# Optimization experiments

Hardware: AMD Instinct MI355X
Metric: run time of the kernel (lower is better)

The kernel has to match this reference:

```python
import jax, jax.numpy as jnp
import numpy as np
import math

N_COARSE, N_FINE = 8192, 32768
DEC_DIM, ENC_DIM, OUT_DIM, K = 256, 128, 128, 16
LN_EPS = 1e-5


def setup_inputs() -> dict:
    key = jax.random.key(0)
    ks = jax.random.split(key, 16)
    s = lambda fan_in: 1.0 / math.sqrt(fan_in)
    return {
        "decoder_features": jax.random.normal(ks[0], (N_COARSE, DEC_DIM), jnp.float32),
        "decoder_pos": jax.random.normal(ks[1], (N_COARSE, 3), jnp.float32),
        "encoder_features": jax.random.normal(ks[2], (N_FINE, ENC_DIM), jnp.float32),
        "encoder_pos": jax.random.normal(ks[3], (N_FINE, 3), jnp.float32),
        "encoder_labels": jax.random.randint(ks[4], (N_FINE,), 0, 13, jnp.int64),
        # params (torch nn.Linear default init scale)
        "Wq": jax.random.uniform(ks[5], (DEC_DIM, ENC_DIM), jnp.float32, -s(ENC_DIM), s(ENC_DIM)),
        "bq": jnp.zeros((DEC_DIM,), jnp.float32),
        "Wk": jax.random.uniform(ks[6], (DEC_DIM, DEC_DIM), jnp.float32, -s(DEC_DIM), s(DEC_DIM)),
        "bk": jnp.zeros((DEC_DIM,), jnp.float32),
        "Wv": jax.random.uniform(ks[7], (DEC_DIM, DEC_DIM), jnp.float32, -s(DEC_DIM), s(DEC_DIM)),
        "bv": jnp.zeros((DEC_DIM,), jnp.float32),
        "W1": jax.random.uniform(ks[8], (OUT_DIM, DEC_DIM + ENC_DIM), jnp.float32, -s(DEC_DIM + ENC_DIM), s(DEC_DIM + ENC_DIM)),
        "b1": jnp.zeros((OUT_DIM,), jnp.float32),
        "W2": jax.random.uniform(ks[9], (OUT_DIM, OUT_DIM), jnp.float32, -s(OUT_DIM), s(OUT_DIM)),
        "b2": jnp.zeros((OUT_DIM,), jnp.float32),
        "ln_g": jnp.ones((OUT_DIM,), jnp.float32),
        "ln_b": jnp.zeros((OUT_DIM,), jnp.float32),
    }


def _knn_indices(encoder_pos, decoder_pos, k):
    # For each fine (encoder) point, k nearest coarse (decoder) points.
    # squared distances [N_fine, N_coarse]
    d2 = (
        jnp.sum(encoder_pos * encoder_pos, axis=1, keepdims=True)
        - 2.0 * encoder_pos @ decoder_pos.T
        + jnp.sum(decoder_pos * decoder_pos, axis=1)[None, :]
    )
    _, idx = jax.lax.top_k(-d2, k)  # [N_fine, K]
    return idx


def reference(decoder_features, decoder_pos, encoder_features, encoder_pos,
              encoder_labels, Wq, bq, Wk, bk, Wv, bv, W1, b1, W2, b2, ln_g, ln_b):
    idx = _knn_indices(encoder_pos, decoder_pos, K)            # [Nf, K]
    nbr = decoder_features[idx]                                 # [Nf, K, Dd]
    query = encoder_features @ Wq.T + bq                        # [Nf, Dd]
    keys = nbr @ Wk.T + bk                                      # [Nf, K, Dd]
    values = nbr @ Wv.T + bv                                    # [Nf, K, Dd]
    scores = jnp.einsum('nd,nkd->nk', query, keys) / math.sqrt(DEC_DIM)
    # segment softmax over edges grouped by fine target == softmax over K
    weights = jax.nn.softmax(scores, axis=-1)                   # [Nf, K]
    agg = jnp.einsum('nk,nkd->nd', weights, values)             # [Nf, Dd]
    combined = jnp.concatenate([agg, encoder_features], axis=-1)
    h = jax.nn.relu(combined @ W1.T + b1)
    up = h @ W2.T + b2                                          # [Nf, out]
    mu = jnp.mean(up, axis=-1, keepdims=True)
    var = jnp.var(up, axis=-1, keepdims=True)
    out = (up - mu) * jax.lax.rsqrt(var + LN_EPS) * ln_g + ln_b
    # dropout is identity in eval mode
    return (out, encoder_pos, encoder_labels)
```

## Files before the change

### kernel.cpp

```cpp
#include <hip/hip_runtime.h>
#include <hip/hip_bf16.h>

typedef __hip_bfloat16 bf16;
typedef unsigned short u16;
typedef float f32x2 __attribute__((ext_vector_type(2)));

#define NC 8192
#define NF 32768
#define KNN 16
#define FMAXV 3.402823466e+38f

__device__ __forceinline__ float bfbits2f(u16 u){
  union { unsigned u; float f; } x; x.u = ((unsigned)u) << 16; return x.f;
}
__device__ __forceinline__ float asfloat(unsigned u){
  union { unsigned u; float f; } x; x.u = u; return x.f;
}
__device__ __forceinline__ f32x2 pk_fma(f32x2 a, f32x2 b, f32x2 c){
  f32x2 d;
  asm("v_pk_fma_f32 %0, %1, %2, %3" : "=v"(d) : "v"(a), "v"(b), "v"(c));
  return d;
}

__global__ __launch_bounds__(256) void k_prep(const float* __restrict__ dpos,
                                              const float* __restrict__ W1,
                                              const float* __restrict__ W2,
                                              float4* __restrict__ posP,
                                              float4* __restrict__ W1eSa,
                                              float4* __restrict__ W1eSb,
                                              float4* __restrict__ W2Sa,
                                              float4* __restrict__ W2Sb){
  int g = blockIdx.x * 256 + threadIdx.x;
  if (g < 4096){
    const float2* dp2 = (const float2*)(dpos + (size_t)g * 6);
    float2 a = dp2[0], b = dp2[1], c = dp2[2];
    float x0 = a.x, y0 = a.y, z0 = b.x;
    float x1 = b.y, y1 = c.x, z1 = c.y;
    float dd0 = __fadd_rn(__fadd_rn(__fmul_rn(x0,x0), __fmul_rn(y0,y0)), __fmul_rn(z0,z0));
    float dd1 = __fadd_rn(__fadd_rn(__fmul_rn(x1,x1), __fmul_rn(y1,y1)), __fmul_rn(z1,z1));
    posP[g * 2]     = make_float4(x0, x1, y0, y1);
    posP[g * 2 + 1] = make_float4(z0, z1, dd0 * 0.5f, dd1 * 0.5f);
  } else if (g >= 8192 && g < 10240){
    int f = g - 8192; int c4 = f >> 6, jg = f & 63;
    W1eSa[f] = ((const float4*)(W1 + (size_t)(2 * jg) * 384 + 256))[c4];
  } else if (g >= 10240 && g < 12288){
    int f = g - 10240; int c4 = f >> 6, jg = f & 63;
    W1eSb[f] = ((const float4*)(W1 + (size_t)(2 * jg + 1) * 384 + 256))[c4];
  } else if (g >= 12288 && g < 14336){
    int f = g - 12288; int c4 = f >> 6, jg = f & 63;
    W2Sa[f] = ((const float4*)(W2 + (size_t)(2 * jg) * 128))[c4];
  } else if (g >= 14336){
    int f = g - 14336; int c4 = f >> 6, jg = f & 63;
    W2Sb[f] = ((const float4*)(W2 + (size_t)(2 * jg + 1) * 128))[c4];
  }
}

__global__ __launch_bounds__(256) void k_wprod(const float* __restrict__ Wk,
                                               const float* __restrict__ Wv,
                                               const float* __restrict__ Wq,
                                               const float* __restrict__ W1,
                                               const float* __restrict__ bk,
                                               const float* __restrict__ bv,
                                               const float* __restrict__ bq,
                                               float* __restrict__ WkqS,
                                               float* __restrict__ WvuS,
                                               float* __restrict__ bkq,
                                               float* __restrict__ bvu,
                                               float* __restrict__ wbq,
                                               float* __restrict__ sbq){
  __shared__ float partial[256];
  __shared__ float red[256];
  int B = blockIdx.x, t = threadIdx.x;
  int csel = B >> 2, tch = B & 3;
  int o = (t & 63) + tch * 64;
  int q = t >> 6;
  int j0 = q * 64;
  if (csel < 128){
    int c = csel;
    float acc = 0.f;
    for (int j = j0; j < j0 + 64; ++j)
      acc = fmaf(Wk[(size_t)j * 256 + o], Wq[(size_t)j * 128 + c], acc);
    partial[t] = acc;
    if (tch == 0) red[t] = bk[t] * Wq[(size_t)t * 128 + c];
    __syncthreads();
    if (t < 64){
      float a = partial[t] + partial[t + 64] + partial[t + 128] + partial[t + 192];
      WkqS[(size_t)((o >> 2) * 128 + c) * 4 + (o & 3)] = a;
    }
    if (tch == 0){
      for (int s = 128; s > 0; s >>= 1){ if (t < s) red[t] += red[t + s]; __syncthreads(); }
      if (t == 0) bkq[c] = red[0];
    }
  } else if (csel < 256){
    int h = csel - 128;
    float acc = 0.f;
    for (int j = j0; j < j0 + 64; ++j)
      acc = fmaf(Wv[(size_t)j * 256 + o], W1[(size_t)h * 384 + j], acc);
    partial[t] = acc;
    if (tch == 0) red[t] = bv[t] * W1[(size_t)h * 384 + t];
    __syncthreads();
    if (t < 64){
      float a = partial[t] + partial[t + 64] + partial[t + 128] + partial[t + 192];
      WvuS[(size_t)((o >> 2) * 128 + h) * 4 + (o & 3)] = a;
    }
    if (tch == 0){
      for (int s = 128; s > 0; s >>= 1){ if (t < s) red[t] += red[t + s]; __syncthreads(); }
      if (t == 0) bvu[h] = red[0];
    }
  } else {
    float acc = 0.f;
    for (int j = j0; j < j0 + 64; ++j)
      acc = fmaf(Wk[(size_t)j * 256 + o], bq[j], acc);
    partial[t] = acc;
    if (tch == 0) red[t] = bk[t] * bq[t];
    __syncthreads();
    if (t < 64){
      float a = partial[t] + partial[t + 64] + partial[t + 128] + partial[t + 192];
      wbq[o] = a;
    }
    if (tch == 0){
      for (int s = 128; s > 0; s >>= 1){ if (t < s) red[t] += red[t + s]; __syncthreads(); }
      if (t == 0) sbq[0] = red[0];
    }
  }
}

__global__ __launch_bounds__(256) void k_dec(const float* __restrict__ df,
                                             const float4* __restrict__ WkqS,
                                             const float4* __restrict__ WvuS,
                                             const float* __restrict__ bkq,
                                             const float* __restrict__ bvu,
                                             const float* __restrict__ wbq,
                                             const float* __restrict__ sbq,
                                             bf16* __restrict__ Zd, bf16* __restrict__ Ud,
                                             float* __restrict__ bqK){
  __shared__ float part[8][32];
  int t = threadIdx.x;
  int g0 = blockIdx.x * 8;
  int half = __builtin_amdgcn_readfirstlane(t >> 7);
  int c = t & 127;
  const float4* W = half ? WvuS : WkqS;
  float acc[8];
  #pragma unroll
  for (int p = 0; p < 8; ++p) acc[p] = 0.f;
  for (int j4 = 0; j4 < 64; ++j4){
    float4 w = W[j4 * 128 + c];
    #pragma unroll
    for (int p = 0; p < 8; ++p){
      float4 a = ((const float4*)(df + (size_t)(g0 + p) * 256))[j4];
      acc[p] += w.x*a.x + w.y*a.y + w.z*a.z + w.w*a.w;
    }
  }
  float bias = half ? bvu[c] : bkq[c];
  bf16* dst = half ? Ud : Zd;
  #pragma unroll
  for (int p = 0; p < 8; ++p)
    dst[(size_t)(g0 + p) * 128 + c] = __float2bfloat16(acc[p] + bias);
  {
    int r = t >> 5, seg = t & 31;
    float s = 0.f;
    const float* dr = df + (size_t)(g0 + r) * 256 + seg * 8;
    const float* wq = wbq + seg * 8;
    #pragma unroll
    for (int e = 0; e < 8; ++e) s = fmaf(dr[e], wq[e], s);
    part[r][seg] = s;
  }
  __syncthreads();
  if (t < 8){
    float s = sbq[0];
    #pragma unroll
    for (int seg = 0; seg < 32; ++seg) s += part[t][seg];
    bqK[g0 + t] = s;
  }
}

__global__ __launch_bounds__(128) void k_attn(const float* __restrict__ epos,
                                              const float4* __restrict__ posP,
                                              const float* __restrict__ ef,
                                              const bf16* __restrict__ Zd,
                                              const bf16* __restrict__ Ud,
                                              const float* __restrict__ bqK,
                                              bf16* __restrict__ hagg){
  __shared__ float lval[2][8][64];
  __shared__ int   lidx[2][8][64];
  __shared__ int   cntL[2][8];

  int t = threadIdx.x, lane = t & 63, w = t >> 6;
  int n0 = blockIdx.x * 16 + w * 8;

  f32x2 nex2[8], ney2[8], nez2[8];
  #pragma unroll
  for (int p = 0; p < 8; ++p){
    float nx = -epos[(n0 + p) * 3 + 0];
    float ny = -epos[(n0 + p) * 3 + 1];
    float nz = -epos[(n0 + p) * 3 + 2];
    nex2[p].x = nx; nex2[p].y = nx;
    ney2[p].x = ny; ney2[p].y = ny;
    nez2[p].x = nz; nez2[p].y = nz;
  }

  f32x2 vmin2[8];
  #pragma unroll
  for (int p = 0; p < 8; ++p){ vmin2[p].x = FMAXV; vmin2[p].y = FMAXV; }
  #pragma unroll 2
  for (int s = 0; s < 64; ++s){
    int q2 = (s * 64 + lane) * 2;
    float4 XY = posP[q2], ZW = posP[q2 + 1];
    f32x2 X = {XY.x, XY.y}, Y = {XY.z, XY.w}, Z = {ZW.x, ZW.y}, W = {ZW.z, ZW.w};
    #pragma unroll
    for (int p = 0; p < 8; ++p){
      f32x2 v2 = pk_fma(nex2[p], X, W);
      v2 = pk_fma(ney2[p], Y, v2);
      v2 = pk_fma(nez2[p], Z, v2);
      vmin2[p].x = fminf(vmin2[p].x, v2.x);
      vmin2[p].y = fminf(vmin2[p].y, v2.y);
    }
  }
  float vmin[8];
  #pragma unroll
  for (int p = 0; p < 8; ++p) vmin[p] = fminf(vmin2[p].x, vmin2[p].y);

  #pragma unroll
  for (int k = 2; k <= 64; k <<= 1){
    #pragma unroll
    for (int j = k >> 1; j > 0; j >>= 1){
      bool keepmin = ((lane & j) == 0) == ((lane & k) == 0);
      #pragma unroll
      for (int p = 0; p < 8; ++p){
        float pv = __shfl_xor(vmin[p], j);
        vmin[p] = keepmin ? fminf(vmin[p], pv) : fmaxf(vmin[p], pv);
      }
    }
  }
  float tau0[8];
  #pragma unroll
  for (int p = 0; p < 8; ++p) tau0[p] = __shfl(vmin[p], 16);

  unsigned long long lmlt = (1ull << lane) - 1ull;
  int cnt[8] = {0,0,0,0,0,0,0,0};
  #pragma unroll 2
  for (int s = 0; s < 64; ++s){
    int q = s * 64 + lane;
    float4 XY = posP[q * 2], ZW = posP[q * 2 + 1];
    f32x2 X = {XY.x, XY.y}, Y = {XY.z, XY.w}, Z = {ZW.x, ZW.y}, W = {ZW.z, ZW.w};
    int cand0 = q * 2;
    #pragma unroll
    for (int p = 0; p < 8; ++p){
      f32x2 v2 = pk_fma(nex2[p], X, W);
      v2 = pk_fma(ney2[p], Y, v2);
      v2 = pk_fma(nez2[p], Z, v2);
      bool h0 = v2.x <= tau0[p];
      bool h1 = v2.y <= tau0[p];
      if (__any(h0 || h1)){
        unsigned long long m0 = __ballot(h0);
        unsigned long long m1 = __ballot(h1);
        int base = cnt[p];
        int c0 = __popcll(m0);
        if (h0){
          int s0 = base + (int)__popcll(m0 & lmlt);
          if (s0 < 64){ lval[w][p][s0] = v2.x; lidx[w][p][s0] = cand0; }
        }
        if (h1){
          int s1 = base + c0 + (int)__popcll(m1 & lmlt);
          if (s1 < 64){ lval[w][p][s1] = v2.y; lidx[w][p][s1] = cand0 + 1; }
        }
        cnt[p] = base + c0 + (int)__popcll(m1);
      }
    }
  }
  if (lane == 0){
    #pragma unroll
    for (int p = 0; p < 8; ++p) cntL[w][p] = cnt[p];
  }
  __syncthreads();

  #pragma unroll 1
  for (int u = 0; u < 4; ++u){
    int p0 = u * 2, p1 = u * 2 + 1;
    int nA = n0 + p0, nB = n0 + p1;
    int c0 = cntL[w][p0]; if (c0 > 64) c0 = 64;
    int c1 = cntL[w][p1]; if (c1 > 64) c1 = 64;
    float va = (lane < c0) ? lval[w][p0][lane] : FMAXV;
    int   ia = (lane < c0) ? lidx[w][p0][lane] : 0x7fffffff;
    float vb = (lane < c1) ? lval[w][p1][lane] : FMAXV;
    int   ib = (lane < c1) ? lidx[w][p1][lane] : 0x7fffffff;

    #pragma unroll
    for (int k = 2; k <= 16; k <<= 1){
      #pragma unroll
      for (int j = k >> 1; j > 0; j >>= 1){
        bool keepmin = ((lane & k) == 0) == ((lane & j) == 0);
        { float pv = __shfl_xor(va, j); int pid = __shfl_xor(ia, j);
          bool pl = (pv < va) || (pv == va && pid < ia);
          if (keepmin ? pl : !pl){ va = pv; ia = pid; } }
        { float pv = __shfl_xor(vb, j); int pid = __shfl_xor(ib, j);
          bool pl = (pv < vb) || (pv == vb && pid < ib);
          if (keepmin ? pl : !pl){ vb = pv; ib = pid; } }
      }
    }
    { float pv = __shfl_xor(va, 16); int pid = __shfl_xor(ia, 16);
      if ((pv < va) || (pv == va && pid < ia)){ va = pv; ia = pid; } }
    { float pv = __shfl_xor(vb, 16); int pid = __shfl_xor(ib, 16);
      if ((pv < vb) || (pv == vb && pid < ib)){ vb = pv; ib = pid; } }
    #pragma unroll
    for (int j = 8; j > 0; j >>= 1){
      bool keepmin = ((lane & 32) == 0) == ((lane & j) == 0);
      { float pv = __shfl_xor(va, j); int pid = __shfl_xor(ia, j);
        bool pl = (pv < va) || (pv == va && pid < ia);
        if (keepmin ? pl : !pl){ va = pv; ia = pid; } }
      { float pv = __shfl_xor(vb, j); int pid = __shfl_xor(ib, j);
        bool pl = (pv < vb) || (pv == vb && pid < ib);
        if (keepmin ? pl : !pl){ vb = pv; ib = pid; } }
    }
    { float pv = __shfl_xor(va, 32); int pid = __shfl_xor(ia, 32);
      if ((pv < va) || (pv == va && pid < ia)){ va = pv; ia = pid; } }
    { float pv = __shfl_xor(vb, 32); int pid = __shfl_xor(ib, 32);
      if ((pv < vb) || (pv == vb && pid < ib)){ vb = pv; ib = pid; } }
    int topi0 = ia, topi1 = ib;

    int kk = lane & 15, part = lane >> 4;
    int ik0 = __shfl(topi0, kk);
    int ik1 = __shfl(topi1, kk);
    const uint4*  zr0 = (const uint4*)((const u16*)Zd + (size_t)ik0 * 128) + part * 4;
    const uint4*  zr1 = (const uint4*)((const u16*)Zd + (size_t)ik1 * 128) + part * 4;
    const float4* e40 = (const float4*)(ef + (size_t)nA * 128) + part * 8;
    const float4* e41 = (const float4*)(ef + (size_t)nB * 128) + part * 8;
    float pr0 = 0.f, pr1 = 0.f;
    #pragma unroll
    for (int i = 0; i < 4; ++i){
      uint4 z0 = zr0[i], z1 = zr1[i];
      float4 ea0 = e40[2 * i], eb0 = e40[2 * i + 1];
      float4 ea1 = e41[2 * i], eb1 = e41[2 * i + 1];
      pr0 = fmaf(ea0.x, asfloat(z0.x << 16), pr0); pr0 = fmaf(ea0.y, asfloat(z0.x & 0xffff0000u), pr0);
      pr0 = fmaf(ea0.z, asfloat(z0.y << 16), pr0); pr0 = fmaf(ea0.w, asfloat(z0.y & 0xffff0000u), pr0);
      pr0 = fmaf(eb0.x, asfloat(z0.z << 16), pr0); pr0 = fmaf(eb0.y, asfloat(z0.z & 0xffff0000u), pr0);
      pr0 = fmaf(eb0.z, asfloat(z0.w << 16), pr0); pr0 = fmaf(eb0.w, asfloat(z0.w & 0xffff0000u), pr0);
      pr1 = fmaf(ea1.x, asfloat(z1.x << 16), pr1); pr1 = fmaf(ea1.y, asfloat(z1.x & 0xffff0000u), pr1);
      pr1 = fmaf(ea1.z, asfloat(z1.y << 16), pr1); pr1 = fmaf(ea1.w, asfloat(z1.y & 0xffff0000u), pr1);
      pr1 = fmaf(eb1.x, asfloat(z1.z << 16), pr1); pr1 = fmaf(eb1.y, asfloat(z1.z & 0xffff0000u), pr1);
      pr1 = fmaf(eb1.z, asfloat(z1.w << 16), pr1); pr1 = fmaf(eb1.w, asfloat(z1.w & 0xffff0000u), pr1);
    }
    pr0 += __shfl_xor(pr0, 16); pr1 += __shfl_xor(pr1, 16);
    pr0 += __shfl_xor(pr0, 32); pr1 += __shfl_xor(pr1, 32);
    float sc0 = (pr0 + bqK[ik0]) * (1.0f / 16.0f);
    float sc1 = (pr1 + bqK[ik1]) * (1.0f / 16.0f);

    float mx0 = sc0, mx1 = sc1;
    #pragma unroll
    for (int off = 8; off >= 1; off >>= 1){
      mx0 = fmaxf(mx0, __shfl_xor(mx0, off));
      mx1 = fmaxf(mx1, __shfl_xor(mx1, off));
    }
    float e0 = (lane < KNN) ? __expf(sc0 - mx0) : 0.f;
    float e1 = (lane < KNN) ? __expf(sc1 - mx1) : 0.f;
    float l0 = e0, l1 = e1;
    #pragma unroll
    for (int off = 8; off >= 1; off >>= 1){
      l0 += __shfl_xor(l0, off);
      l1 += __shfl_xor(l1, off);
    }
    float wgt0 = (lane < KNN) ? (e0 / l0) : 0.f;
    float wgt1 = (lane < KNN) ? (e1 / l1) : 0.f;

    float a00 = 0.f, a01 = 0.f, a10 = 0.f, a11 = 0.f;
    #pragma unroll
    for (int k = 0; k < KNN; ++k){
      int ikk0 = __shfl(topi0, k);
      int ikk1 = __shfl(topi1, k);
      float wk0 = __shfl(wgt0, k);
      float wk1 = __shfl(wgt1, k);
      ushort2 u0 = *(const ushort2*)((const u16*)Ud + (size_t)ikk0 * 128 + lane * 2);
      ushort2 u1 = *(const ushort2*)((const u16*)Ud + (size_t)ikk1 * 128 + lane * 2);
      a00 = fmaf(wk0, bfbits2f(u0.x), a00);
      a01 = fmaf(wk0, bfbits2f(u0.y), a01);
      a10 = fmaf(wk1, bfbits2f(u1.x), a10);
      a11 = fmaf(wk1, bfbits2f(u1.y), a11);
    }
    bf16 h00 = __float2bfloat16(a00), h01 = __float2bfloat16(a01);
    bf16 h10 = __float2bfloat16(a10), h11 = __float2bfloat16(a11);
    ushort2 st0; st0.x = *(u16*)&h00; st0.y = *(u16*)&h01;
    ushort2 st1; st1.x = *(u16*)&h10; st1.y = *(u16*)&h11;
    *(ushort2*)(hagg + (size_t)nA * 128 + lane * 2) = st0;
    *(ushort2*)(hagg + (size_t)nB * 128 + lane * 2) = st1;
  }
}

__global__ __launch_bounds__(256) void k_mlp(const bf16* __restrict__ hagg,
                                             const float* __restrict__ ef,
                                             const float4* __restrict__ W1eSa,
                                             const float4* __restrict__ W1eSb,
                                             const float* __restrict__ b1,
                                             const float4* __restrict__ W2Sa,
                                             const float4* __restrict__ W2Sb,
                                             const float* __restrict__ b2,
                                             const float* __restrict__ lng, const float* __restrict__ lnb,
                                             const float* __restrict__ epos, const int* __restrict__ lab,
                                             float* __restrict__ out){
  __shared__ float hbuf[16 * 128];
  __shared__ float ubuf[16 * 128];
  __shared__ float stats[32];
  int t = threadIdx.x;
  int n0 = blockIdx.x * 16;
  {
    int gid = blockIdx.x * 256 + t;
    if (gid < NF){
      float* op = out + (size_t)NF * 128;
      op[gid * 3 + 0] = epos[gid * 3 + 0];
      op[gid * 3 + 1] = epos[gid * 3 + 1];
      op[gid * 3 + 2] = epos[gid * 3 + 2];
      out[(size_t)NF * 128 + (size_t)NF * 3 + gid] = (float)lab[gid];
    }
  }
  int jg = t & 63;
  int pg4 = __builtin_amdgcn_readfirstlane((t >> 6) * 4);
  int j0 = jg * 2;
  float acc[2][4];
  #pragma unroll
  for (int a = 0; a < 2; ++a)
    #pragma unroll
    for (int p = 0; p < 4; ++p) acc[a][p] = 0.f;
  for (int c4 = 0; c4 < 32; ++c4){
    float4 wa = W1eSa[c4 * 64 + jg];
    float4 wb = W1eSb[c4 * 64 + jg];
    #pragma unroll
    for (int p = 0; p < 4; ++p){
      float4 x = ((const float4*)(ef + (size_t)(n0 + pg4 + p) * 128))[c4];
      acc[0][p] += wa.x*x.x + wa.y*x.y + wa.z*x.z + wa.w*x.w;
      acc[1][p] += wb.x*x.x + wb.y*x.y + wb.z*x.z + wb.w*x.w;
    }
  }
  float b1a = b1[j0], b1b = b1[j0 + 1];
  #pragma unroll
  for (int p = 0; p < 4; ++p){
    size_t row = (size_t)(n0 + pg4 + p);
    ushort2 hgv = *(const ushort2*)((const u16*)hagg + row * 128 + j0);
    hbuf[(pg4 + p) * 128 + j0]     = fmaxf(acc[0][p] + b1a + bfbits2f(hgv.x), 0.f);
    hbuf[(pg4 + p) * 128 + j0 + 1] = fmaxf(acc[1][p] + b1b + bfbits2f(hgv.y), 0.f);
  }
  __syncthreads();
  float acc2[2][4];
  #pragma unroll
  for (int a = 0; a < 2; ++a)
    #pragma unroll
    for (int p = 0; p < 4; ++p) acc2[a][p] = 0.f;
  const float4* hb4 = (const float4*)hbuf;
  for (int c4 = 0; c4 < 32; ++c4){
    float4 wa = W2Sa[c4 * 64 + jg];
    float4 wb = W2Sb[c4 * 64 + jg];
    #pragma unroll
    for (int p = 0; p < 4; ++p){
      float4 x = hb4[(pg4 + p) * 32 + c4];
      acc2[0][p] += wa.x*x.x + wa.y*x.y + wa.z*x.z + wa.w*x.w;
      acc2[1][p] += wb.x*x.x + wb.y*x.y + wb.z*x.z + wb.w*x.w;
    }
  }
  float b2a = b2[j0], b2b = b2[j0 + 1];
  float u[2][4];
  #pragma unroll
  for (int p = 0; p < 4; ++p){
    u[0][p] = acc2[0][p] + b2a;
    u[1][p] = acc2[1][p] + b2b;
    ubuf[(pg4 + p) * 128 + j0]     = u[0][p];
    ubuf[(pg4 + p) * 128 + j0 + 1] = u[1][p];
  }
  __syncthreads();
  {
    int p = t >> 4, qi = t & 15;
    const float* ub = &ubuf[p * 128 + qi * 8];
    float s = 0.f, s2 = 0.f;
    #pragma unroll
    for (int e2i = 0; e2i < 8; ++e2i){ float v = ub[e2i]; s += v; s2 += v * v; }
    #pragma unroll
    for (int off = 1; off < 16; off <<= 1){ s += __shfl_xor(s, off); s2 += __shfl_xor(s2, off); }
    if (qi == 0){
      float mu = s * (1.f / 128.f);
      float var = s2 * (1.f / 128.f) - mu * mu;
      stats[p] = mu;
      stats[16 + p] = rsqrtf(fmaxf(var, 0.f) + 1e-5f);
    }
  }
  __syncthreads();
  float ga = lng[j0], gb = lng[j0 + 1];
  float ba = lnb[j0], bbv = lnb[j0 + 1];
  #pragma unroll
  for (int p = 0; p < 4; ++p){
    float mu = stats[pg4 + p], rs = stats[16 + pg4 + p];
    out[(size_t)(n0 + pg4 + p) * 128 + j0]     = (u[0][p] - mu) * rs * ga + ba;
    out[(size_t)(n0 + pg4 + p) * 128 + j0 + 1] = (u[1][p] - mu) * rs * gb + bbv;
  }
}

extern "C" void kernel_launch(void* const* d_in, const int* in_sizes, int n_in,
                              void* d_out, int out_size, void* d_ws, size_t ws_size,
                              hipStream_t stream){
  const float* df   = (const float*)d_in[0];
  const float* dpos = (const float*)d_in[1];
  const float* ef   = (const float*)d_in[2];
  const float* epos = (const float*)d_in[3];
  const int*   lab  = (const int*)d_in[4];
  const float* Wq = (const float*)d_in[5];
  const float* bq = (const float*)d_in[6];
  const float* Wk = (const float*)d_in[7];
  const float* bk = (const float*)d_in[8];
  const float* Wv = (const float*)d_in[9];
  const float* bv = (const float*)d_in[10];
  const float* W1 = (const float*)d_in[11];
  const float* b1 = (const float*)d_in[12];
  const float* W2 = (const float*)d_in[13];
  const float* b2 = (const float*)d_in[14];
  const float* lng = (const float*)d_in[15];
  const float* lnb = (const float*)d_in[16];
  float* out = (float*)d_out;

  char* wsb = (char*)d_ws;
  float4* posP  = (float4*)(wsb);
  bf16*   Zd    = (bf16*)(wsb + 131072);
  bf16*   Ud    = (bf16*)(wsb + 2228224);
  float*  bqK   = (float*)(wsb + 4325376);
  bf16*   hagg  = (bf16*)(wsb + 4358144);
  float4* W1eSa = (float4*)(wsb + 12746752);
  float4* W1eSb = (float4*)(wsb + 12779520);
  float4* W2Sa  = (float4*)(wsb + 12812288);
  float4* W2Sb  = (float4*)(wsb + 12845056);
  float*  WkqS  = (float*)(wsb + 12877824);
  float*  WvuS  = (float*)(wsb + 13008896);
  float*  bkq   = (float*)(wsb + 13139968);
  float*  bvu   = (float*)(wsb + 13140480);
  float*  wbq   = (float*)(wsb + 13140992);
  float*  sbq   = (float*)(wsb + 13142016);

  k_prep  <<<64,   256, 0, stream>>>(dpos, W1, W2, posP, W1eSa, W1eSb, W2Sa, W2Sb);
  k_wprod <<<1028, 256, 0, stream>>>(Wk, Wv, Wq, W1, bk, bv, bq, WkqS, WvuS, bkq, bvu, wbq, sbq);
  k_dec   <<<NC / 8, 256, 0, stream>>>(df, (const float4*)WkqS, (const float4*)WvuS, bkq, bvu, wbq, sbq, Zd, Ud, bqK);
  k_attn  <<<NF / 16, 128, 0, stream>>>(epos, posP, ef, Zd, Ud, bqK, hagg);
  k_mlp   <<<NF / 16, 256, 0, stream>>>(hagg, ef, W1eSa, W1eSb, b1, W2Sa, W2Sb, b2, lng, lnb, epos, lab, out);
  (void)in_sizes; (void)n_in; (void)out_size; (void)ws_size;
}
```

Measured before the change: 360.9 us.

## Split KNN across four waves per point group and fuse attention into MLP kernel

The KNN kernel now has each of four waves scan a quarter of the coarse points for the same 8 fine points. Per-wave minima are merged through LDS to form the pruning threshold, and candidates are collected with shared-memory atomics. The top-16 indices go to a workspace buffer, and the attention score, softmax and value aggregation move into the MLP kernel, which keeps the aggregate in LDS in fp32 instead of writing a bf16 intermediate. This shortens each wave's serial scan and raises parallelism, at the cost of an extra cross-wave merge, LDS atomic contention and redundant ef reads in the fused kernel.

```diff
diff --git a/kernel.cpp b/kernel.cpp
--- a/kernel.cpp
+++ b/kernel.cpp
@@ -174,20 +174,17 @@
   }
 }
 
-__global__ __launch_bounds__(128) void k_attn(const float* __restrict__ epos,
-                                              const float4* __restrict__ posP,
-                                              const float* __restrict__ ef,
-                                              const bf16* __restrict__ Zd,
-                                              const bf16* __restrict__ Ud,
-                                              const float* __restrict__ bqK,
-                                              bf16* __restrict__ hagg){
-  __shared__ float lval[2][8][64];
-  __shared__ int   lidx[2][8][64];
-  __shared__ int   cntL[2][8];
+__global__ __launch_bounds__(256) void k_knn(const float* __restrict__ epos,
+                                             const float4* __restrict__ posP,
+                                             int* __restrict__ knnI){
+  __shared__ float smin[8 * 64];
+  __shared__ float tauLDS[8];
+  __shared__ int   cnt[8];
+  __shared__ float lval[8][64];
+  __shared__ int   lidx[8][64];
 
   int t = threadIdx.x, lane = t & 63, w = t >> 6;
-  int n0 = blockIdx.x * 16 + w * 8;
-
+  int n0 = blockIdx.x * 8;
   f32x2 nex2[8], ney2[8], nez2[8];
   #pragma unroll
   for (int p = 0; p < 8; ++p){
@@ -198,14 +195,15 @@
     ney2[p].x = ny; ney2[p].y = ny;
     nez2[p].x = nz; nez2[p].y = nz;
   }
+  const float4* base = posP + w * 2048;
 
   f32x2 vmin2[8];
   #pragma unroll
   for (int p = 0; p < 8; ++p){ vmin2[p].x = FMAXV; vmin2[p].y = FMAXV; }
   #pragma unroll 2
-  for (int s = 0; s < 64; ++s){
+  for (int s = 0; s < 16; ++s){
     int q2 = (s * 64 + lane) * 2;
-    float4 XY = posP[q2], ZW = posP[q2 + 1];
+    float4 XY = base[q2], ZW = base[q2 + 1];
     f32x2 X = {XY.x, XY.y}, Y = {XY.z, XY.w}, Z = {ZW.x, ZW.y}, W = {ZW.z, ZW.w};
     #pragma unroll
     for (int p = 0; p < 8; ++p){
@@ -232,58 +230,68 @@
       }
     }
   }
+  if (lane < 16){
+    #pragma unroll
+    for (int p = 0; p < 8; ++p) smin[p * 64 + w * 16 + lane] = vmin[p];
+  }
+  if (t < 8) cnt[t] = 0;
+  __syncthreads();
+
+  {
+    int src = (lane & 16) ? (lane ^ 15) : lane;
+    float v0 = smin[(w * 2 + 0) * 64 + src];
+    float v1 = smin[(w * 2 + 1) * 64 + src];
+    #pragma unroll
+    for (int j = 16; j > 0; j >>= 1){
+      bool keepmin = ((lane & 32) == 0) == ((lane & j) == 0);
+      float p0 = __shfl_xor(v0, j); v0 = keepmin ? fminf(v0, p0) : fmaxf(v0, p0);
+      float p1 = __shfl_xor(v1, j); v1 = keepmin ? fminf(v1, p1) : fmaxf(v1, p1);
+    }
+    #pragma unroll
+    for (int j = 32; j > 0; j >>= 1){
+      bool keepmin = ((lane & j) == 0);
+      float p0 = __shfl_xor(v0, j); v0 = keepmin ? fminf(v0, p0) : fmaxf(v0, p0);
+      float p1 = __shfl_xor(v1, j); v1 = keepmin ? fminf(v1, p1) : fmaxf(v1, p1);
+    }
+    if (lane == 16){ tauLDS[w * 2] = v0; tauLDS[w * 2 + 1] = v1; }
+  }
+  __syncthreads();
   float tau0[8];
   #pragma unroll
-  for (int p = 0; p < 8; ++p) tau0[p] = __shfl(vmin[p], 16);
-
-  unsigned long long lmlt = (1ull << lane) - 1ull;
-  int cnt[8] = {0,0,0,0,0,0,0,0};
+  for (int p = 0; p < 8; ++p) tau0[p] = tauLDS[p];
+
   #pragma unroll 2
-  for (int s = 0; s < 64; ++s){
+  for (int s = 0; s < 16; ++s){
     int q = s * 64 + lane;
-    float4 XY = posP[q * 2], ZW = posP[q * 2 + 1];
+    float4 XY = base[q * 2], ZW = base[q * 2 + 1];
     f32x2 X = {XY.x, XY.y}, Y = {XY.z, XY.w}, Z = {ZW.x, ZW.y}, W = {ZW.z, ZW.w};
-    int cand0 = q * 2;
+    int cand0 = w * 2048 + q * 2;
     #pragma unroll
     for (int p = 0; p < 8; ++p){
       f32x2 v2 = pk_fma(nex2[p], X, W);
       v2 = pk_fma(ney2[p], Y, v2);
       v2 = pk_fma(nez2[p], Z, v2);
-      bool h0 = v2.x <= tau0[p];
-      bool h1 = v2.y <= tau0[p];
-      if (__any(h0 || h1)){
-        unsigned long long m0 = __ballot(h0);
-        unsigned long long m1 = __ballot(h1);
-        int base = cnt[p];
-        int c0 = __popcll(m0);
-        if (h0){
-          int s0 = base + (int)__popcll(m0 & lmlt);
-          if (s0 < 64){ lval[w][p][s0] = v2.x; lidx[w][p][s0] = cand0; }
-        }
-        if (h1){
-          int s1 = base + c0 + (int)__popcll(m1 & lmlt);
-          if (s1 < 64){ lval[w][p][s1] = v2.y; lidx[w][p][s1] = cand0 + 1; }
-        }
-        cnt[p] = base + c0 + (int)__popcll(m1);
+      if (v2.x <= tau0[p]){
+        int slot = atomicAdd(&cnt[p], 1);
+        if (slot < 64){ lval[p][slot] = v2.x; lidx[p][slot] = cand0; }
       }
-    }
-  }
-  if (lane == 0){
-    #pragma unroll
-    for (int p = 0; p < 8; ++p) cntL[w][p] = cnt[p];
-  }
-  __syncthreads();
-
-  #pragma unroll 1
-  for (int u = 0; u < 4; ++u){
-    int p0 = u * 2, p1 = u * 2 + 1;
+      if (v2.y <= tau0[p]){
+        int slot = atomicAdd(&cnt[p], 1);
+        if (slot < 64){ lval[p][slot] = v2.y; lidx[p][slot] = cand0 + 1; }
+      }
+    }
+  }
+  __syncthreads();
+
+  {
+    int p0 = w * 2, p1 = w * 2 + 1;
     int nA = n0 + p0, nB = n0 + p1;
-    int c0 = cntL[w][p0]; if (c0 > 64) c0 = 64;
-    int c1 = cntL[w][p1]; if (c1 > 64) c1 = 64;
-    float va = (lane < c0) ? lval[w][p0][lane] : FMAXV;
-    int   ia = (lane < c0) ? lidx[w][p0][lane] : 0x7fffffff;
-    float vb = (lane < c1) ? lval[w][p1][lane] : FMAXV;
-    int   ib = (lane < c1) ? lidx[w][p1][lane] : 0x7fffffff;
+    int c0 = cnt[p0]; if (c0 > 64) c0 = 64;
+    int c1 = cnt[p1]; if (c1 > 64) c1 = 64;
+    float va = (lane < c0) ? lval[p0][lane] : FMAXV;
+    int   ia = (lane < c0) ? lidx[p0][lane] : 0x7fffffff;
+    float vb = (lane < c1) ? lval[p1][lane] : FMAXV;
+    int   ib = (lane < c1) ? lidx[p1][lane] : 0x7fffffff;
 
     #pragma unroll
     for (int k = 2; k <= 16; k <<= 1){
@@ -316,91 +324,35 @@
       if ((pv < va) || (pv == va && pid < ia)){ va = pv; ia = pid; } }
     { float pv = __shfl_xor(vb, 32); int pid = __shfl_xor(ib, 32);
       if ((pv < vb) || (pv == vb && pid < ib)){ vb = pv; ib = pid; } }
-    int topi0 = ia, topi1 = ib;
-
-    int kk = lane & 15, part = lane >> 4;
-    int ik0 = __shfl(topi0, kk);
-    int ik1 = __shfl(topi1, kk);
-    const uint4*  zr0 = (const uint4*)((const u16*)Zd + (size_t)ik0 * 128) + part * 4;
-    const uint4*  zr1 = (const uint4*)((const u16*)Zd + (size_t)ik1 * 128) + part * 4;
-    const float4* e40 = (const float4*)(ef + (size_t)nA * 128) + part * 8;
-    const float4* e41 = (const float4*)(ef + (size_t)nB * 128) + part * 8;
-    float pr0 = 0.f, pr1 = 0.f;
-    #pragma unroll
-    for (int i = 0; i < 4; ++i){
-      uint4 z0 = zr0[i], z1 = zr1[i];
-      float4 ea0 = e40[2 * i], eb0 = e40[2 * i + 1];
-      float4 ea1 = e41[2 * i], eb1 = e41[2 * i + 1];
-      pr0 = fmaf(ea0.x, asfloat(z0.x << 16), pr0); pr0 = fmaf(ea0.y, asfloat(z0.x & 0xffff0000u), pr0);
-      pr0 = fmaf(ea0.z, asfloat(z0.y << 16), pr0); pr0 = fmaf(ea0.w, asfloat(z0.y & 0xffff0000u), pr0);
-      pr0 = fmaf(eb0.x, asfloat(z0.z << 16), pr0); pr0 = fmaf(eb0.y, asfloat(z0.z & 0xffff0000u), pr0);
-      pr0 = fmaf(eb0.z, asfloat(z0.w << 16), pr0); pr0 = fmaf(eb0.w, asfloat(z0.w & 0xffff0000u), pr0);
-      pr1 = fmaf(ea1.x, asfloat(z1.x << 16), pr1); pr1 = fmaf(ea1.y, asfloat(z1.x & 0xffff0000u), pr1);
-      pr1 = fmaf(ea1.z, asfloat(z1.y << 16), pr1); pr1 = fmaf(ea1.w, asfloat(z1.y & 0xffff0000u), pr1);
-      pr1 = fmaf(eb1.x, asfloat(z1.z << 16), pr1); pr1 = fmaf(eb1.y, asfloat(z1.z & 0xffff0000u), pr1);
-      pr1 = fmaf(eb1.z, asfloat(z1.w << 16), pr1); pr1 = fmaf(eb1.w, asfloat(z1.w & 0xffff0000u), pr1);
-    }
-    pr0 += __shfl_xor(pr0, 16); pr1 += __shfl_xor(pr1, 16);
-    pr0 += __shfl_xor(pr0, 32); pr1 += __shfl_xor(pr1, 32);
-    float sc0 = (pr0 + bqK[ik0]) * (1.0f / 16.0f);
-    float sc1 = (pr1 + bqK[ik1]) * (1.0f / 16.0f);
-
-    float mx0 = sc0, mx1 = sc1;
-    #pragma unroll
-    for (int off = 8; off >= 1; off >>= 1){
-      mx0 = fmaxf(mx0, __shfl_xor(mx0, off));
-      mx1 = fmaxf(mx1, __shfl_xor(mx1, off));
-    }
-    float e0 = (lane < KNN) ? __expf(sc0 - mx0) : 0.f;
-    float e1 = (lane < KNN) ? __expf(sc1 - mx1) : 0.f;
-    float l0 = e0, l1 = e1;
-    #pragma unroll
-    for (int off = 8; off >= 1; off >>= 1){
-      l0 += __shfl_xor(l0, off);
-      l1 += __shfl_xor(l1, off);
-    }
-    float wgt0 = (lane < KNN) ? (e0 / l0) : 0.f;
-    float wgt1 = (lane < KNN) ? (e1 / l1) : 0.f;
-
-    float a00 = 0.f, a01 = 0.f, a10 = 0.f, a11 = 0.f;
-    #pragma unroll
-    for (int k = 0; k < KNN; ++k){
-      int ikk0 = __shfl(topi0, k);
-      int ikk1 = __shfl(topi1, k);
-      float wk0 = __shfl(wgt0, k);
-      float wk1 = __shfl(wgt1, k);
-      ushort2 u0 = *(const ushort2*)((const u16*)Ud + (size_t)ikk0 * 128 + lane * 2);
-      ushort2 u1 = *(const ushort2*)((const u16*)Ud + (size_t)ikk1 * 128 + lane * 2);
-      a00 = fmaf(wk0, bfbits2f(u0.x), a00);
-      a01 = fmaf(wk0, bfbits2f(u0.y), a01);
-      a10 = fmaf(wk1, bfbits2f(u1.x), a10);
-      a11 = fmaf(wk1, bfbits2f(u1.y), a11);
-    }
-    bf16 h00 = __float2bfloat16(a00), h01 = __float2bfloat16(a01);
-    bf16 h10 = __float2bfloat16(a10), h11 = __float2bfloat16(a11);
-    ushort2 st0; st0.x = *(u16*)&h00; st0.y = *(u16*)&h01;
-    ushort2 st1; st1.x = *(u16*)&h10; st1.y = *(u16*)&h11;
-    *(ushort2*)(hagg + (size_t)nA * 128 + lane * 2) = st0;
-    *(ushort2*)(hagg + (size_t)nB * 128 + lane * 2) = st1;
-  }
-}
-
-__global__ __launch_bounds__(256) void k_mlp(const bf16* __restrict__ hagg,
-                                             const float* __restrict__ ef,
-                                             const float4* __restrict__ W1eSa,
-                                             const float4* __restrict__ W1eSb,
-                                             const float* __restrict__ b1,
-                                             const float4* __restrict__ W2Sa,
-                                             const float4* __restrict__ W2Sb,
-                                             const float* __restrict__ b2,
-                                             const float* __restrict__ lng, const float* __restrict__ lnb,
-                                             const float* __restrict__ epos, const int* __restrict__ lab,
-                                             float* __restrict__ out){
+
+    if (lane < 16){
+      knnI[(size_t)nA * 16 + lane] = ia;
+      knnI[(size_t)nB * 16 + lane] = ib;
+    }
+  }
+}
+
+__global__ __launch_bounds__(256) void k_amlp(const int* __restrict__ knnI,
+                                              const bf16* __restrict__ Zd,
+                                              const bf16* __restrict__ Ud,
+                                              const float* __restrict__ bqK,
+                                              const float* __restrict__ ef,
+                                              const float4* __restrict__ W1eSa,
+                                              const float4* __restrict__ W1eSb,
+                                              const float* __restrict__ b1,
+                                              const float4* __restrict__ W2Sa,
+                                              const float4* __restrict__ W2Sb,
+                                              const float* __restrict__ b2,
+                                              const float* __restrict__ lng, const float* __restrict__ lnb,
+                                              const float* __restrict__ epos, const int* __restrict__ lab,
+                                              float* __restrict__ out){
+  __shared__ float haggL[16 * 128];
   __shared__ float hbuf[16 * 128];
   __shared__ float ubuf[16 * 128];
   __shared__ float stats[32];
   int t = threadIdx.x;
   int n0 = blockIdx.x * 16;
+  int lane = t & 63, w = t >> 6;
   {
     int gid = blockIdx.x * 256 + t;
     if (gid < NF){
@@ -411,6 +363,58 @@
       out[(size_t)NF * 128 + (size_t)NF * 3 + gid] = (float)lab[gid];
     }
   }
+
+  {
+    int kk = lane & 15;
+    int pp = w * 4 + (lane >> 4);
+    int n = n0 + pp;
+    int ik = knnI[(size_t)n * 16 + kk];
+    const uint4*  zr = (const uint4*)((const u16*)Zd + (size_t)ik * 128);
+    const float4* e4 = (const float4*)(ef + (size_t)n * 128);
+    float pr = 0.f;
+    #pragma unroll
+    for (int i = 0; i < 16; ++i){
+      uint4 z = zr[i];
+      float4 ea = e4[2 * i], eb = e4[2 * i + 1];
+      pr = fmaf(ea.x, asfloat(z.x << 16), pr); pr = fmaf(ea.y, asfloat(z.x & 0xffff0000u), pr);
+      pr = fmaf(ea.z, asfloat(z.y << 16), pr); pr = fmaf(ea.w, asfloat(z.y & 0xffff0000u), pr);
+      pr = fmaf(eb.x, asfloat(z.z << 16), pr); pr = fmaf(eb.y, asfloat(z.z & 0xffff0000u), pr);
+      pr = fmaf(eb.z, asfloat(z.w << 16), pr); pr = fmaf(eb.w, asfloat(z.w & 0xffff0000u), pr);
+    }
+    float sc = (pr + bqK[ik]) * (1.0f / 16.0f);
+    float mx = sc;
+    #pragma unroll
+    for (int off = 1; off < 16; off <<= 1) mx = fmaxf(mx, __shfl_xor(mx, off));
+    float e = __expf(sc - mx);
+    float l = e;
+    #pragma unroll
+    for (int off = 1; off < 16; off <<= 1) l += __shfl_xor(l, off);
+    float wgt = e / l;
+
+    float acc8[8];
+    #pragma unroll
+    for (int j = 0; j < 8; ++j) acc8[j] = 0.f;
+    int gbase = lane & 48;
+    #pragma unroll
+    for (int k2 = 0; k2 < 16; ++k2){
+      int src = gbase | k2;
+      float wk = __shfl(wgt, src);
+      int ikk = __shfl(ik, src);
+      uint4 uu = *(const uint4*)((const u16*)Ud + (size_t)ikk * 128 + kk * 8);
+      acc8[0] = fmaf(wk, asfloat(uu.x << 16), acc8[0]);
+      acc8[1] = fmaf(wk, asfloat(uu.x & 0xffff0000u), acc8[1]);
+      acc8[2] = fmaf(wk, asfloat(uu.y << 16), acc8[2]);
+      acc8[3] = fmaf(wk, asfloat(uu.y & 0xffff0000u), acc8[3]);
+      acc8[4] = fmaf(wk, asfloat(uu.z << 16), acc8[4]);
+      acc8[5] = fmaf(wk, asfloat(uu.z & 0xffff0000u), acc8[5]);
+      acc8[6] = fmaf(wk, asfloat(uu.w << 16), acc8[6]);
+      acc8[7] = fmaf(wk, asfloat(uu.w & 0xffff0000u), acc8[7]);
+    }
+    float4* hp = (float4*)&haggL[pp * 128 + kk * 8];
+    hp[0] = make_float4(acc8[0], acc8[1], acc8[2], acc8[3]);
+    hp[1] = make_float4(acc8[4], acc8[5], acc8[6], acc8[7]);
+  }
+
   int jg = t & 63;
   int pg4 = __builtin_amdgcn_readfirstlane((t >> 6) * 4);
   int j0 = jg * 2;
@@ -429,13 +433,13 @@
       acc[1][p] += wb.x*x.x + wb.y*x.y + wb.z*x.z + wb.w*x.w;
     }
   }
+  __syncthreads();
   float b1a = b1[j0], b1b = b1[j0 + 1];
   #pragma unroll
   for (int p = 0; p < 4; ++p){
-    size_t row = (size_t)(n0 + pg4 + p);
-    ushort2 hgv = *(const ushort2*)((const u16*)hagg + row * 128 + j0);
-    hbuf[(pg4 + p) * 128 + j0]     = fmaxf(acc[0][p] + b1a + bfbits2f(hgv.x), 0.f);
-    hbuf[(pg4 + p) * 128 + j0 + 1] = fmaxf(acc[1][p] + b1b + bfbits2f(hgv.y), 0.f);
+    float2 hgv = *(const float2*)&haggL[(pg4 + p) * 128 + j0];
+    hbuf[(pg4 + p) * 128 + j0]     = fmaxf(acc[0][p] + b1a + hgv.x, 0.f);
+    hbuf[(pg4 + p) * 128 + j0 + 1] = fmaxf(acc[1][p] + b1b + hgv.y, 0.f);
   }
   __syncthreads();
   float acc2[2][4];
@@ -517,7 +521,7 @@
   bf16*   Zd    = (bf16*)(wsb + 131072);
   bf16*   Ud    = (bf16*)(wsb + 2228224);
   float*  bqK   = (float*)(wsb + 4325376);
-  bf16*   hagg  = (bf16*)(wsb + 4358144);
+  int*    knnI  = (int*)(wsb + 4358144);
   float4* W1eSa = (float4*)(wsb + 12746752);
   float4* W1eSb = (float4*)(wsb + 12779520);
   float4* W2Sa  = (float4*)(wsb + 12812288);
@@ -532,7 +536,7 @@
   k_prep  <<<64,   256, 0, stream>>>(dpos, W1, W2, posP, W1eSa, W1eSb, W2Sa, W2Sb);
   k_wprod <<<1028, 256, 0, stream>>>(Wk, Wv, Wq, W1, bk, bv, bq, WkqS, WvuS, bkq, bvu, wbq, sbq);
   k_dec   <<<NC / 8, 256, 0, stream>>>(df, (const float4*)WkqS, (const float4*)WvuS, bkq, bvu, wbq, sbq, Zd, Ud, bqK);
-  k_attn  <<<NF / 16, 128, 0, stream>>>(epos, posP, ef, Zd, Ud, bqK, hagg);
-  k_mlp   <<<NF / 16, 256, 0, stream>>>(hagg, ef, W1eSa, W1eSb, b1, W2Sa, W2Sb, b2, lng, lnb, epos, lab, out);
+  k_knn   <<<NF / 8, 256, 0, stream>>>(epos, posP, knnI);
+  k_amlp  <<<NF / 16, 256, 0, stream>>>(knnI, Zd, Ud, bqK, ef, W1eSa, W1eSb, b1, W2Sa, W2Sb, b2, lng, lnb, epos, lab, out);
   (void)in_sizes; (void)n_in; (void)out_size; (void)ws_size;
 }
```

Result: faster. 339.7 us (-5.9%).
